# Kernel tuning notes

Hardware: AMD Instinct MI355X
Metric: run time of the kernel (lower is better)

## Reference

```python
import jax, jax.numpy as jnp
import numpy as np

N_NODES = 100000
N_EDGES = 1600000
N_REL = 8
IN_CH = 64
HIDDEN = 64
OUT_CH = 32


def setup_inputs() -> dict:
    key = jax.random.key(0)
    ks = jax.random.split(key, 10)
    s_in = 1.0 / np.sqrt(IN_CH)
    s_h = 1.0 / np.sqrt(HIDDEN)
    return {
        "x": jax.random.normal(ks[0], (N_NODES, IN_CH), dtype=jnp.float32),
        "edge_index": jax.random.randint(ks[1], (2, N_EDGES), 0, N_NODES, dtype=jnp.int64),
        "edge_type": jax.random.randint(ks[2], (N_EDGES,), 0, N_REL, dtype=jnp.int64),
        "W0": jax.random.normal(ks[3], (N_REL, IN_CH, HIDDEN), dtype=jnp.float32) * s_in,
        "Q0": jax.random.normal(ks[4], (HIDDEN, 1), dtype=jnp.float32) * s_h,
        "K0": jax.random.normal(ks[5], (HIDDEN, 1), dtype=jnp.float32) * s_h,
        "b0": jnp.zeros((HIDDEN,), dtype=jnp.float32),
        "W1": jax.random.normal(ks[6], (N_REL, HIDDEN, OUT_CH), dtype=jnp.float32) * s_h,
        "Q1": jax.random.normal(ks[7], (OUT_CH, 1), dtype=jnp.float32) * (1.0 / np.sqrt(OUT_CH)),
        "K1": jax.random.normal(ks[8], (OUT_CH, 1), dtype=jnp.float32) * (1.0 / np.sqrt(OUT_CH)),
        "b1": jnp.zeros((OUT_CH,), dtype=jnp.float32),
    }


def rgat_conv(x, src, dst, et, W, Q, K, b, n_nodes):
    # relation-typed transform of all nodes: [R, N, out]
    xw = jnp.einsum("ni,rio->rno", x, W)
    # per-node, per-relation attention logits (heads=1, dim=1)
    q = jnp.einsum("rno,od->rnd", xw, Q)[..., 0]  # [R, N]
    k = jnp.einsum("rno,od->rnd", xw, K)[..., 0]  # [R, N]
    # additive self-attention, leaky_relu slope 0.2 (PyG RGATConv default)
    alpha = jax.nn.leaky_relu(q[et, dst] + k[et, src], negative_slope=0.2)  # [E]
    # across-relation segment softmax over incoming edges of each dst node
    amax = jax.ops.segment_max(alpha, dst, num_segments=n_nodes)
    a = jnp.exp(alpha - amax[dst])
    denom = jax.ops.segment_sum(a, dst, num_segments=n_nodes)
    a = a / (denom[dst] + 1e-16)
    # weighted scatter-add aggregation of transformed source features
    msg = a[:, None] * xw[et, src]  # [E, out]
    return jax.ops.segment_sum(msg, dst, num_segments=n_nodes) + b


def reference(x, edge_index, edge_type, W0, Q0, K0, b0, W1, Q1, K1, b1):
    src, dst = edge_index[0], edge_index[1]
    n = x.shape[0]
    h = rgat_conv(x, src, dst, edge_type, W0, Q0, K0, b0, n)
    h = jax.nn.relu(h)  # dropout p=0.0 -> identity
    out = rgat_conv(h, src, dst, edge_type, W1, Q1, K1, b1, n)
    return out
```

## Files before the change

### kernel.cpp

```cpp
#include <hip/hip_runtime.h>
#include <hip/hip_bf16.h>
#include <math.h>


#define CSR_CHUNK 8192

__global__ void k_bhist(const int* __restrict__ dst, int* __restrict__ bcount,
                        int E, int NB) {
    __shared__ int h[512];
    int t = threadIdx.x;
    for (int i = t; i < NB; i += 256) h[i] = 0;
    __syncthreads();
    int e0 = blockIdx.x * CSR_CHUNK;
    int e1 = min(e0 + CSR_CHUNK, E);
    for (int i = e0 + t; i < e1; i += 256) atomicAdd(&h[dst[i] >> 8], 1);
    __syncthreads();
    for (int i = t; i < NB; i += 256) {
        int c = h[i];
        if (c) atomicAdd(&bcount[i], c);
    }
}

__global__ void k_bscan(const int* __restrict__ bcount, int* __restrict__ bstart,
                        int* __restrict__ gcur, int* __restrict__ rowptr,
                        int NB, int N, int E) {
    __shared__ int s[512];
    int t = threadIdx.x;
    int v = (t < NB) ? bcount[t] : 0;
    s[t] = v;
    __syncthreads();
    for (int off = 1; off < 512; off <<= 1) {
        int a = (t >= off) ? s[t - off] : 0;
        __syncthreads();
        s[t] += a;
        __syncthreads();
    }
    int excl = s[t] - v;
    if (t < NB) {
        bstart[t] = excl;
        gcur[t] = excl;
    }
    if (t == 0) {
        bstart[NB] = E;
        rowptr[N] = E;
    }
}

__global__ void k_bscatter(const int* __restrict__ src, const int* __restrict__ dst,
                           const int* __restrict__ et, int* __restrict__ gcur,
                           unsigned* __restrict__ ebuf, int E, int NB) {
    __shared__ int h[512];
    __shared__ int basearr[512];
    int t = threadIdx.x;
    for (int i = t; i < NB; i += 256) h[i] = 0;
    __syncthreads();
    int e0 = blockIdx.x * CSR_CHUNK;
    int e1 = min(e0 + CSR_CHUNK, E);
    for (int i = e0 + t; i < e1; i += 256) atomicAdd(&h[dst[i] >> 8], 1);
    __syncthreads();
    for (int i = t; i < NB; i += 256) {
        int c = h[i];
        basearr[i] = c ? atomicAdd(&gcur[i], c) : 0;
        h[i] = 0;
    }
    __syncthreads();
    for (int i = e0 + t; i < e1; i += 256) {
        int d = dst[i];
        int b = d >> 8;
        int off = atomicAdd(&h[b], 1);
        ebuf[basearr[b] + off] =
            ((unsigned)(d & 255) << 20) | ((unsigned)et[i] << 17) | (unsigned)src[i];
    }
}

__global__ void k_bsort(const unsigned* __restrict__ ebuf, const int* __restrict__ bstart,
                        int* __restrict__ rowptr, int* __restrict__ csr, int N) {
    __shared__ int lh[2048];
    __shared__ int ls[2048];
    __shared__ int ss[256];
    int b = blockIdx.x, t = threadIdx.x;
    int e0 = bstart[b], e1 = bstart[b + 1];
    for (int i = t; i < 2048; i += 256) lh[i] = 0;
    __syncthreads();
    for (int i = e0 + t; i < e1; i += 256) {
        unsigned u = ebuf[i];
        atomicAdd(&lh[(int)(((u >> 20) & 255) * 8 + ((u >> 17) & 7))], 1);
    }
    __syncthreads();
    int loc[8];
    int s = 0;
#pragma unroll
    for (int j = 0; j < 8; j++) {
        loc[j] = s;
        s += lh[t * 8 + j];
    }
    ss[t] = s;
    __syncthreads();
    for (int off = 1; off < 256; off <<= 1) {
        int a = (t >= off) ? ss[t - off] : 0;
        __syncthreads();
        ss[t] += a;
        __syncthreads();
    }
    int excl = ss[t] - s;
#pragma unroll
    for (int j = 0; j < 8; j++) ls[t * 8 + j] = excl + loc[j];
    int node = b * 256 + t;
    if (node < N) rowptr[node] = e0 + excl;
    __syncthreads();
    for (int i = t; i < 2048; i += 256) lh[i] = 0;
    __syncthreads();
    for (int i = e0 + t; i < e1; i += 256) {
        unsigned u = ebuf[i];
        int key = (int)(((u >> 20) & 255) * 8 + ((u >> 17) & 7));
        int off = atomicAdd(&lh[key], 1);
        csr[e0 + ls[key] + off] = (int)(u & 0xFFFFF);
    }
}


__global__ void k_wt2(const float* __restrict__ W, __hip_bfloat16* __restrict__ hi,
                      __hip_bfloat16* __restrict__ lo, int OUT, int total) {
    int t = blockIdx.x * blockDim.x + threadIdx.x;
    if (t < total) {
        int per = 64 * OUT;
        int r = t / per;
        int rem = t % per;
        int i = rem / OUT;
        int o = rem % OUT;
        float v = W[t];
        __hip_bfloat16 h = __float2bfloat16(v);
        __hip_bfloat16 l = __float2bfloat16(v - __bfloat162float(h));
        size_t idx = (size_t)o * 512 + i * 8 + r;
        hi[idx] = h;
        lo[idx] = l;
    }
}

__global__ void k_wqk(const float* W, const float* Qv, const float* Kv,
                      float* wq, float* wk, int OUT) {
    int t = blockIdx.x * blockDim.x + threadIdx.x;
    if (t < 8 * 64) {
        int r = t >> 6, i = t & 63;
        const float* wrow = W + ((size_t)r * 64 + i) * OUT;
        float a = 0.f, b = 0.f;
        for (int o = 0; o < OUT; o++) {
            float w = wrow[o];
            a += w * Qv[o];
            b += w * Kv[o];
        }
        wq[t] = a;
        wk[t] = b;
    }
}

__global__ __launch_bounds__(256) void k_qk2(
        const float* __restrict__ xin, const float* __restrict__ wq,
        const float* __restrict__ wk, float* __restrict__ qn,
        float* __restrict__ kn, unsigned short* __restrict__ xbb, int N) {
    __shared__ float xt[64][65];
    __shared__ float swq[8 * 65], swk[8 * 65];
    int t = threadIdx.x;
    int nb0 = blockIdx.x * 64;
    for (int i = t; i < 512; i += 256) {
        int r = i >> 6, c = i & 63;
        swq[r * 65 + c] = wq[i];
        swk[r * 65 + c] = wk[i];
    }
    for (int i = t; i < 1024; i += 256) {
        int ns = i >> 4;
        int c4 = i & 15;
        int n = nb0 + ns;
        float4 v = {0.f, 0.f, 0.f, 0.f};
        if (n < N) v = ((const float4*)xin)[(size_t)n * 16 + c4];
        xt[ns][c4 * 4 + 0] = v.x;
        xt[ns][c4 * 4 + 1] = v.y;
        xt[ns][c4 * 4 + 2] = v.z;
        xt[ns][c4 * 4 + 3] = v.w;
        if (n < N) {
            __hip_bfloat16 b0 = __float2bfloat16(v.x);
            __hip_bfloat16 b1 = __float2bfloat16(v.y);
            __hip_bfloat16 b2 = __float2bfloat16(v.z);
            __hip_bfloat16 b3 = __float2bfloat16(v.w);
            ushort4 o;
            o.x = *(unsigned short*)&b0;
            o.y = *(unsigned short*)&b1;
            o.z = *(unsigned short*)&b2;
            o.w = *(unsigned short*)&b3;
            *(ushort4*)(xbb + (size_t)n * 64 + c4 * 4) = o;
        }
    }
    __syncthreads();
#pragma unroll
    for (int g = t; g < 512; g += 256) {
        int ns = g >> 3, r = g & 7;
        int n = nb0 + ns;
        if (n < N) {
            float qa = 0.f, ka = 0.f;
#pragma unroll
            for (int i = 0; i < 64; i++) {
                float xv = xt[ns][i];
                qa += xv * swq[r * 65 + i];
                ka += xv * swk[r * 65 + i];
            }
            qn[(size_t)n * 8 + r] = qa;
            kn[(size_t)n * 8 + r] = ka;
        }
    }
}

#define ZSTR 520
template <int OUT, bool RELU>
__global__ __launch_bounds__(256) void k_fused(
        const int* __restrict__ rowptr, const int* __restrict__ csr,
        const float* __restrict__ qn, const float* __restrict__ kn,
        const unsigned short* __restrict__ xb,
        const __hip_bfloat16* __restrict__ wthi,
        const __hip_bfloat16* __restrict__ wtlo,
        const float* __restrict__ bias, float* __restrict__ xout, int N) {
    using v8s = __attribute__((ext_vector_type(8))) short;
    using v4f = __attribute__((ext_vector_type(4))) float;
    __shared__ unsigned short zt[16 * ZSTR];
    int wv = threadIdx.x >> 6;
    int lane = threadIdx.x & 63;
    int nb0 = blockIdx.x * 16;

    for (int q = 0; q < 4; q++) {
        int nl = wv * 4 + q;
        int wid = nb0 + nl;
        uint4 pack = {0u, 0u, 0u, 0u};
        if (wid < N) {
            int r0 = rowptr[wid], r1 = rowptr[wid + 1];
            float qv = (lane < 8) ? qn[wid * 8 + lane] : 0.f;
            float denom = 0.f;
            float a0 = 0.f, a1 = 0.f, a2 = 0.f, a3 = 0.f;
            float a4 = 0.f, a5 = 0.f, a6 = 0.f, a7 = 0.f;
            int currel = 0;
            float racc = 0.f;

            for (int base = r0; base < r1; base += 64) {
                int s = base + lane;
                int pk = (s < r1) ? csr[s] : 0;
                int src = pk & 0x1FFFF;
                int rel = pk >> 17;
                float qq = __shfl(qv, rel, 64);
                float tv = 0.f;
                if (s < r1) {
                    float v = qq + kn[src * 8 + rel];
                    v = (v >= 0.f) ? v : 0.2f * v;
                    tv = __expf(v);
                }
                float ts = tv;
#pragma unroll
                for (int off = 32; off > 0; off >>= 1) ts += __shfl_xor(ts, off, 64);
                denom += ts;

                int cnt = min(64, r1 - base);
                int tvi = (int)__float_as_uint(tv);
                for (int j = 0; j < cnt; j += 16) {
                    unsigned p[16];
                    float t[16];
#pragma unroll
                    for (int u = 0; u < 16; u++) {
                        p[u] = (unsigned)__builtin_amdgcn_readlane(pk, j + u);
                        t[u] = __uint_as_float(
                            (unsigned)__builtin_amdgcn_readlane(tvi, j + u));
                    }
                    unsigned xu[16];
#pragma unroll
                    for (int u = 0; u < 16; u++)
                        xu[u] = (unsigned)xb[(size_t)(p[u] & 0x1FFFF) * 64 + lane];
#pragma unroll
                    for (int u = 0; u < 16; u++) {
                        int rl = (int)(p[u] >> 17);
                        if (rl != currel) {
                            switch (currel) {
                                case 0: a0 += racc; break;
                                case 1: a1 += racc; break;
                                case 2: a2 += racc; break;
                                case 3: a3 += racc; break;
                                case 4: a4 += racc; break;
                                case 5: a5 += racc; break;
                                case 6: a6 += racc; break;
                                case 7: a7 += racc; break;
                            }
                            currel = rl;
                            racc = 0.f;
                        }
                        racc += t[u] * __uint_as_float(xu[u] << 16);
                    }
                }
            }
            switch (currel) {
                case 0: a0 += racc; break;
                case 1: a1 += racc; break;
                case 2: a2 += racc; break;
                case 3: a3 += racc; break;
                case 4: a4 += racc; break;
                case 5: a5 += racc; break;
                case 6: a6 += racc; break;
                case 7: a7 += racc; break;
            }
            float inv = 1.f / (denom + 1e-16f);
            float av[8] = {a0, a1, a2, a3, a4, a5, a6, a7};
            unsigned short u[8];
#pragma unroll
            for (int r = 0; r < 8; r++) {
                __hip_bfloat16 b = __float2bfloat16(av[r] * inv);
                u[r] = *(unsigned short*)&b;
            }
            pack.x = (unsigned)u[0] | ((unsigned)u[1] << 16);
            pack.y = (unsigned)u[2] | ((unsigned)u[3] << 16);
            pack.z = (unsigned)u[4] | ((unsigned)u[5] << 16);
            pack.w = (unsigned)u[6] | ((unsigned)u[7] << 16);
        }
        *(uint4*)&zt[nl * ZSTR + lane * 8] = pack;
    }
    __syncthreads();

    int quad = lane >> 4;
    int l15 = lane & 15;
    int nt = wv;
    if (nt * 16 < OUT) {
        const short* wh = (const short*)wthi;
        const short* wl = (const short*)wtlo;
        v4f acc = {0.f, 0.f, 0.f, 0.f};
#pragma unroll
        for (int k0 = 0; k0 < 512; k0 += 32) {
            int koff = k0 + quad * 8;
            v8s A = *(const v8s*)&zt[l15 * ZSTR + koff];
            v8s bh = *(const v8s*)(wh + (size_t)(nt * 16 + l15) * 512 + koff);
            v8s bl = *(const v8s*)(wl + (size_t)(nt * 16 + l15) * 512 + koff);
            acc = __builtin_amdgcn_mfma_f32_16x16x32_bf16(A, bh, acc, 0, 0, 0);
            acc = __builtin_amdgcn_mfma_f32_16x16x32_bf16(A, bl, acc, 0, 0, 0);
        }
        float bcol = bias[nt * 16 + l15];
#pragma unroll
        for (int g = 0; g < 4; g++) {
            int row = nb0 + quad * 4 + g;
            if (row < N) {
                float o = acc[g] + bcol;
                if (RELU) o = fmaxf(o, 0.f);
                xout[(size_t)row * OUT + nt * 16 + l15] = o;
            }
        }
    }
}


extern "C" void kernel_launch(void* const* d_in, const int* in_sizes, int n_in,
                              void* d_out, int out_size, void* d_ws, size_t ws_size,
                              hipStream_t stream) {
    const float* x   = (const float*)d_in[0];
    const int*   ei  = (const int*)d_in[1];
    const int*   et  = (const int*)d_in[2];
    const float* W0  = (const float*)d_in[3];
    const float* Q0  = (const float*)d_in[4];
    const float* K0  = (const float*)d_in[5];
    const float* b0  = (const float*)d_in[6];
    const float* W1  = (const float*)d_in[7];
    const float* Q1  = (const float*)d_in[8];
    const float* K1  = (const float*)d_in[9];
    const float* b1  = (const float*)d_in[10];
    float* out = (float*)d_out;

    const int N = in_sizes[0] / 64;
    const int E = in_sizes[2];
    const int* src = ei;
    const int* dst = ei + E;
    const int NB = (N + 255) >> 8;

    char* p = (char*)d_ws;
    auto alloc = [&](size_t bytes) -> void* {
        void* r = (void*)p;
        p += ((bytes + 255) / 256) * 256;
        return r;
    };
    int* rowptr   = (int*)alloc((size_t)(N + 1) * 4);
    int* bcount   = (int*)alloc(513 * 4);
    int* bstart   = (int*)alloc(513 * 4);
    int* gcur     = (int*)alloc(513 * 4);
    unsigned* ebuf = (unsigned*)alloc((size_t)E * 4);
    int* csr      = (int*)alloc((size_t)E * 4);
    float* wq     = (float*)alloc(8 * 64 * 4);
    float* wk     = (float*)alloc(8 * 64 * 4);
    float* qn     = (float*)alloc((size_t)N * 8 * 4);
    float* kn     = (float*)alloc((size_t)N * 8 * 4);
    __hip_bfloat16* wthi = (__hip_bfloat16*)alloc((size_t)64 * 512 * 2);
    __hip_bfloat16* wtlo = (__hip_bfloat16*)alloc((size_t)64 * 512 * 2);
    float* h      = (float*)alloc((size_t)N * 64 * 4);
    unsigned short* xbb = (unsigned short*)alloc((size_t)N * 64 * 2);

    int nchunks = (E + CSR_CHUNK - 1) / CSR_CHUNK;
    hipMemsetAsync(bcount, 0, (size_t)NB * 4, stream);
    k_bhist<<<nchunks, 256, 0, stream>>>(dst, bcount, E, NB);
    k_bscan<<<1, 512, 0, stream>>>(bcount, bstart, gcur, rowptr, NB, N, E);
    k_bscatter<<<nchunks, 256, 0, stream>>>(src, dst, et, gcur, ebuf, E, NB);
    k_bsort<<<NB, 256, 0, stream>>>(ebuf, bstart, rowptr, csr, N);

    int nfb = (N + 15) / 16;
    int nqkb = (N + 63) / 64;

    k_wqk<<<2, 256, 0, stream>>>(W0, Q0, K0, wq, wk, 64);
    k_qk2<<<nqkb, 256, 0, stream>>>(x, wq, wk, qn, kn, xbb, N);
    k_wt2<<<(8 * 64 * 64 + 255) / 256, 256, 0, stream>>>(W0, wthi, wtlo, 64, 8 * 64 * 64);
    k_fused<64, true><<<nfb, 256, 0, stream>>>(rowptr, csr, qn, kn, xbb,
                                               wthi, wtlo, b0, h, N);

    k_wqk<<<2, 256, 0, stream>>>(W1, Q1, K1, wq, wk, 32);
    k_qk2<<<nqkb, 256, 0, stream>>>(h, wq, wk, qn, kn, xbb, N);
    k_wt2<<<(8 * 64 * 32 + 255) / 256, 256, 0, stream>>>(W1, wthi, wtlo, 32, 8 * 64 * 32);
    k_fused<32, false><<<nfb, 256, 0, stream>>>(rowptr, csr, qn, kn, xbb,
                                                wthi, wtlo, b1, out, N);
}
```

Measured before the change: 444.9 us.

## Precompute block edge attention weights cooperatively into shared memory before gather

Adds a fast path for 16-node blocks with at most 512 edges. All 256 threads first compute the per-edge attention exponentials and pack them into shared memory, locating each edge's node by binary search over the rowptr slice. Per-node denominators are accumulated with shared-memory atomics. The gather loop then reads the weights uniformly from LDS, so the per-wave 64-edge chunking, reductions and readlanes go away. Blocks with more than 512 edges fall back to the old path. The cost is extra LDS, two more barriers and shared atomics on the denominators.

```diff
diff --git a/kernel.cpp b/kernel.cpp
--- a/kernel.cpp
+++ b/kernel.cpp
@@ -210,6 +210,22 @@
 }
 
 #define ZSTR 520
+#define EMAX 512
+
+#define FLUSH8()                          \
+    do {                                  \
+        switch (currel) {                 \
+            case 0: a0 += racc; break;    \
+            case 1: a1 += racc; break;    \
+            case 2: a2 += racc; break;    \
+            case 3: a3 += racc; break;    \
+            case 4: a4 += racc; break;    \
+            case 5: a5 += racc; break;    \
+            case 6: a6 += racc; break;    \
+            case 7: a7 += racc; break;    \
+        }                                 \
+    } while (0)
+
 template <int OUT, bool RELU>
 __global__ __launch_bounds__(256) void k_fused(
         const int* __restrict__ rowptr, const int* __restrict__ csr,
@@ -221,100 +237,175 @@
     using v8s = __attribute__((ext_vector_type(8))) short;
     using v4f = __attribute__((ext_vector_type(4))) float;
     __shared__ unsigned short zt[16 * ZSTR];
-    int wv = threadIdx.x >> 6;
-    int lane = threadIdx.x & 63;
+    __shared__ uint2 s_rec[EMAX];
+    __shared__ int s_rp[17];
+    __shared__ float s_q[128];
+    __shared__ float s_den[16];
+    int t = threadIdx.x;
+    int wv = t >> 6;
+    int lane = t & 63;
     int nb0 = blockIdx.x * 16;
 
-    for (int q = 0; q < 4; q++) {
-        int nl = wv * 4 + q;
-        int wid = nb0 + nl;
-        uint4 pack = {0u, 0u, 0u, 0u};
-        if (wid < N) {
-            int r0 = rowptr[wid], r1 = rowptr[wid + 1];
-            float qv = (lane < 8) ? qn[wid * 8 + lane] : 0.f;
-            float denom = 0.f;
+    if (t < 17) {
+        int nd = nb0 + t;
+        s_rp[t] = rowptr[nd > N ? N : nd];
+    }
+    if (t < 128) {
+        int nd = nb0 + (t >> 3);
+        s_q[t] = (nd < N) ? qn[(size_t)nd * 8 + (t & 7)] : 0.f;
+    }
+    if (t < 16) s_den[t] = 0.f;
+    __syncthreads();
+    int e0 = s_rp[0];
+    int esz = s_rp[16] - e0;
+
+    if (esz <= EMAX) {
+        for (int i = t; i < esz; i += 256) {
+            int ge = e0 + i;
+            int pk = csr[ge];
+            int lo = 0;
+            lo = (s_rp[lo + 8] <= ge) ? lo + 8 : lo;
+            lo = (s_rp[lo + 4] <= ge) ? lo + 4 : lo;
+            lo = (s_rp[lo + 2] <= ge) ? lo + 2 : lo;
+            lo = (s_rp[lo + 1] <= ge) ? lo + 1 : lo;
+            int rel = pk >> 17;
+            int src = pk & 0x1FFFF;
+            float v = s_q[lo * 8 + rel] + kn[(size_t)src * 8 + rel];
+            v = (v >= 0.f) ? v : 0.2f * v;
+            float tv = __expf(v);
+            atomicAdd(&s_den[lo], tv);
+            s_rec[i] = uint2{__float_as_uint(tv), (unsigned)pk};
+        }
+        __syncthreads();
+
+#pragma unroll 1
+        for (int q = 0; q < 4; q++) {
+            int nl = wv * 4 + q;
+            int r0 = s_rp[nl] - e0;
+            int r1 = s_rp[nl + 1] - e0;
             float a0 = 0.f, a1 = 0.f, a2 = 0.f, a3 = 0.f;
             float a4 = 0.f, a5 = 0.f, a6 = 0.f, a7 = 0.f;
             int currel = 0;
             float racc = 0.f;
-
-            for (int base = r0; base < r1; base += 64) {
-                int s = base + lane;
-                int pk = (s < r1) ? csr[s] : 0;
-                int src = pk & 0x1FFFF;
-                int rel = pk >> 17;
-                float qq = __shfl(qv, rel, 64);
-                float tv = 0.f;
-                if (s < r1) {
-                    float v = qq + kn[src * 8 + rel];
-                    v = (v >= 0.f) ? v : 0.2f * v;
-                    tv = __expf(v);
+#pragma unroll 1
+            for (int j = r0; j < r1; j += 16) {
+                float tvv[16];
+                int pkk[16];
+#pragma unroll
+                for (int u = 0; u < 16; u++) {
+                    int ii = j + u;
+                    bool ok = ii < r1;
+                    ii = ok ? ii : (r1 - 1);
+                    uint2 rc = s_rec[ii];
+                    tvv[u] = __uint_as_float(
+                        __builtin_amdgcn_readfirstlane((int)(ok ? rc.x : 0u)));
+                    pkk[u] = __builtin_amdgcn_readfirstlane((int)rc.y);
                 }
-                float ts = tv;
-#pragma unroll
-                for (int off = 32; off > 0; off >>= 1) ts += __shfl_xor(ts, off, 64);
-                denom += ts;
-
-                int cnt = min(64, r1 - base);
-                int tvi = (int)__float_as_uint(tv);
-                for (int j = 0; j < cnt; j += 16) {
-                    unsigned p[16];
-                    float t[16];
-#pragma unroll
-                    for (int u = 0; u < 16; u++) {
-                        p[u] = (unsigned)__builtin_amdgcn_readlane(pk, j + u);
-                        t[u] = __uint_as_float(
-                            (unsigned)__builtin_amdgcn_readlane(tvi, j + u));
+                unsigned short xu[16];
+#pragma unroll
+                for (int u = 0; u < 16; u++)
+                    xu[u] = xb[(size_t)(pkk[u] & 0x1FFFF) * 64 + lane];
+#pragma unroll
+                for (int u = 0; u < 16; u++) {
+                    int rl = pkk[u] >> 17;
+                    if (rl != currel) {
+                        FLUSH8();
+                        currel = rl;
+                        racc = 0.f;
                     }
-                    unsigned xu[16];
-#pragma unroll
-                    for (int u = 0; u < 16; u++)
-                        xu[u] = (unsigned)xb[(size_t)(p[u] & 0x1FFFF) * 64 + lane];
-#pragma unroll
-                    for (int u = 0; u < 16; u++) {
-                        int rl = (int)(p[u] >> 17);
-                        if (rl != currel) {
-                            switch (currel) {
-                                case 0: a0 += racc; break;
-                                case 1: a1 += racc; break;
-                                case 2: a2 += racc; break;
-                                case 3: a3 += racc; break;
-                                case 4: a4 += racc; break;
-                                case 5: a5 += racc; break;
-                                case 6: a6 += racc; break;
-                                case 7: a7 += racc; break;
+                    racc += tvv[u] * __uint_as_float(((unsigned)xu[u]) << 16);
+                }
+            }
+            FLUSH8();
+            float inv = 1.f / (s_den[nl] + 1e-16f);
+            float av[8] = {a0, a1, a2, a3, a4, a5, a6, a7};
+            unsigned short us[8];
+#pragma unroll
+            for (int r = 0; r < 8; r++) {
+                __hip_bfloat16 b = __float2bfloat16(av[r] * inv);
+                us[r] = *(unsigned short*)&b;
+            }
+            uint4 pack;
+            pack.x = (unsigned)us[0] | ((unsigned)us[1] << 16);
+            pack.y = (unsigned)us[2] | ((unsigned)us[3] << 16);
+            pack.z = (unsigned)us[4] | ((unsigned)us[5] << 16);
+            pack.w = (unsigned)us[6] | ((unsigned)us[7] << 16);
+            *(uint4*)&zt[nl * ZSTR + lane * 8] = pack;
+        }
+    } else {
+        for (int q = 0; q < 4; q++) {
+            int nl = wv * 4 + q;
+            int wid = nb0 + nl;
+            uint4 pack = {0u, 0u, 0u, 0u};
+            if (wid < N) {
+                int r0 = rowptr[wid], r1 = rowptr[wid + 1];
+                float qv = (lane < 8) ? qn[wid * 8 + lane] : 0.f;
+                float denom = 0.f;
+                float a0 = 0.f, a1 = 0.f, a2 = 0.f, a3 = 0.f;
+                float a4 = 0.f, a5 = 0.f, a6 = 0.f, a7 = 0.f;
+                int currel = 0;
+                float racc = 0.f;
+
+                for (int base = r0; base < r1; base += 64) {
+                    int s = base + lane;
+                    int pk = (s < r1) ? csr[s] : 0;
+                    int src = pk & 0x1FFFF;
+                    int rel = pk >> 17;
+                    float qq = __shfl(qv, rel, 64);
+                    float tv = 0.f;
+                    if (s < r1) {
+                        float v = qq + kn[src * 8 + rel];
+                        v = (v >= 0.f) ? v : 0.2f * v;
+                        tv = __expf(v);
+                    }
+                    float ts = tv;
+#pragma unroll
+                    for (int off = 32; off > 0; off >>= 1) ts += __shfl_xor(ts, off, 64);
+                    denom += ts;
+
+                    int cnt = min(64, r1 - base);
+                    int tvi = (int)__float_as_uint(tv);
+                    for (int j = 0; j < cnt; j += 16) {
+                        unsigned p[16];
+                        float tf[16];
+#pragma unroll
+                        for (int u = 0; u < 16; u++) {
+                            p[u] = (unsigned)__builtin_amdgcn_readlane(pk, j + u);
+                            tf[u] = __uint_as_float(
+                                (unsigned)__builtin_amdgcn_readlane(tvi, j + u));
+                        }
+                        unsigned xg[16];
+#pragma unroll
+                        for (int u = 0; u < 16; u++)
+                            xg[u] = (unsigned)xb[(size_t)(p[u] & 0x1FFFF) * 64 + lane];
+#pragma unroll
+                        for (int u = 0; u < 16; u++) {
+                            int rl = (int)(p[u] >> 17);
+                            if (rl != currel) {
+                                FLUSH8();
+                                currel = rl;
+                                racc = 0.f;
                             }
-                            currel = rl;
-                            racc = 0.f;
+                            racc += tf[u] * __uint_as_float(xg[u] << 16);
                         }
-                        racc += t[u] * __uint_as_float(xu[u] << 16);
                     }
                 }
+                FLUSH8();
+                float inv = 1.f / (denom + 1e-16f);
+                float av[8] = {a0, a1, a2, a3, a4, a5, a6, a7};
+                unsigned short us[8];
+#pragma unroll
+                for (int r = 0; r < 8; r++) {
+                    __hip_bfloat16 b = __float2bfloat16(av[r] * inv);
+                    us[r] = *(unsigned short*)&b;
+                }
+                pack.x = (unsigned)us[0] | ((unsigned)us[1] << 16);
+                pack.y = (unsigned)us[2] | ((unsigned)us[3] << 16);
+                pack.z = (unsigned)us[4] | ((unsigned)us[5] << 16);
+                pack.w = (unsigned)us[6] | ((unsigned)us[7] << 16);
             }
-            switch (currel) {
-                case 0: a0 += racc; break;
-                case 1: a1 += racc; break;
-                case 2: a2 += racc; break;
-                case 3: a3 += racc; break;
-                case 4: a4 += racc; break;
-                case 5: a5 += racc; break;
-                case 6: a6 += racc; break;
-                case 7: a7 += racc; break;
-            }
-            float inv = 1.f / (denom + 1e-16f);
-            float av[8] = {a0, a1, a2, a3, a4, a5, a6, a7};
-            unsigned short u[8];
-#pragma unroll
-            for (int r = 0; r < 8; r++) {
-                __hip_bfloat16 b = __float2bfloat16(av[r] * inv);
-                u[r] = *(unsigned short*)&b;
-            }
-            pack.x = (unsigned)u[0] | ((unsigned)u[1] << 16);
-            pack.y = (unsigned)u[2] | ((unsigned)u[3] << 16);
-            pack.z = (unsigned)u[4] | ((unsigned)u[5] << 16);
-            pack.w = (unsigned)u[6] | ((unsigned)u[7] << 16);
-        }
-        *(uint4*)&zt[nl * ZSTR + lane * 8] = pack;
+            *(uint4*)&zt[nl * ZSTR + lane * 8] = pack;
+        }
     }
     __syncthreads();
 
```

Result: no change. 438.3 us, median of 2 (-1.5%).

## Compute attention scores per edge uniformly in gather loop instead of lane-parallel batch

Applied to the files above, without the earlier changes.

The per-node aggregation loop drops the 64-lane batched attention computation with cross-lane reductions and readlane broadcasts. It now reads 16 CSR entries as uniform (scalar) loads, fetches their k values, and computes the exp weights redundantly in every lane alongside the feature gather. The denominator is accumulated inline, so the shuffle reductions go away. The CSR build now stores the full packed word, and the zero-fill of the tile moves to the start so out-of-range waves can exit early. The cost is redundant per-lane exp and k loads; the gain is fewer cross-lane operations and less serialization on low-degree nodes.

```diff
diff --git a/kernel.cpp b/kernel.cpp
--- a/kernel.cpp
+++ b/kernel.cpp
@@ -114,7 +114,7 @@
         unsigned u = ebuf[i];
         int key = (int)(((u >> 20) & 255) * 8 + ((u >> 17) & 7));
         int off = atomicAdd(&lh[key], 1);
-        csr[e0 + ls[key] + off] = (int)(u & 0xFFFFF);
+        csr[e0 + ls[key] + off] = (int)u;
     }
 }
 
@@ -210,6 +210,21 @@
 }
 
 #define ZSTR 520
+
+#define FLUSH8()                          \
+    do {                                  \
+        switch (currel) {                 \
+            case 0: a0 += racc; break;    \
+            case 1: a1 += racc; break;    \
+            case 2: a2 += racc; break;    \
+            case 3: a3 += racc; break;    \
+            case 4: a4 += racc; break;    \
+            case 5: a5 += racc; break;    \
+            case 6: a6 += racc; break;    \
+            case 7: a7 += racc; break;    \
+        }                                 \
+    } while (0)
+
 template <int OUT, bool RELU>
 __global__ __launch_bounds__(256) void k_fused(
         const int* __restrict__ rowptr, const int* __restrict__ csr,
@@ -221,106 +236,89 @@
     using v8s = __attribute__((ext_vector_type(8))) short;
     using v4f = __attribute__((ext_vector_type(4))) float;
     __shared__ unsigned short zt[16 * ZSTR];
-    int wv = threadIdx.x >> 6;
-    int lane = threadIdx.x & 63;
+    int t = threadIdx.x;
+    int wvu = __builtin_amdgcn_readfirstlane(t >> 6);
+    int lane = t & 63;
     int nb0 = blockIdx.x * 16;
 
+    {
+        uint4 zz = {0u, 0u, 0u, 0u};
+#pragma unroll
+        for (int q = 0; q < 4; q++)
+            *(uint4*)&zt[(wvu * 4 + q) * ZSTR + lane * 8] = zz;
+    }
+
+#pragma unroll 1
     for (int q = 0; q < 4; q++) {
-        int nl = wv * 4 + q;
-        int wid = nb0 + nl;
-        uint4 pack = {0u, 0u, 0u, 0u};
-        if (wid < N) {
-            int r0 = rowptr[wid], r1 = rowptr[wid + 1];
-            float qv = (lane < 8) ? qn[wid * 8 + lane] : 0.f;
-            float denom = 0.f;
-            float a0 = 0.f, a1 = 0.f, a2 = 0.f, a3 = 0.f;
-            float a4 = 0.f, a5 = 0.f, a6 = 0.f, a7 = 0.f;
-            int currel = 0;
-            float racc = 0.f;
-
-            for (int base = r0; base < r1; base += 64) {
-                int s = base + lane;
-                int pk = (s < r1) ? csr[s] : 0;
-                int src = pk & 0x1FFFF;
-                int rel = pk >> 17;
-                float qq = __shfl(qv, rel, 64);
-                float tv = 0.f;
-                if (s < r1) {
-                    float v = qq + kn[src * 8 + rel];
-                    v = (v >= 0.f) ? v : 0.2f * v;
-                    tv = __expf(v);
+        int wid = nb0 + wvu * 4 + q;
+        if (wid >= N) break;
+        int r0 = rowptr[wid];
+        int r1 = rowptr[wid + 1];
+        int qvec = 0;
+        if (lane < 8) qvec = ((const int*)qn)[wid * 8 + lane];
+
+        float a0 = 0.f, a1 = 0.f, a2 = 0.f, a3 = 0.f;
+        float a4 = 0.f, a5 = 0.f, a6 = 0.f, a7 = 0.f;
+        float racc = 0.f, denom = 0.f;
+        int currel = 0;
+
+#pragma unroll 1
+        for (int j = r0; j < r1; j += 16) {
+            int pk[16];
+            float kv[16];
+            unsigned short xu[16];
+#pragma unroll
+            for (int u = 0; u < 16; u++) {
+                int ii = (j + u < r1) ? (j + u) : (r1 - 1);
+                pk[u] = csr[ii];
+            }
+#pragma unroll
+            for (int u = 0; u < 16; u++) {
+                int s_ = pk[u] & 0x1FFFF;
+                int r_ = (pk[u] >> 17) & 7;
+                kv[u] = kn[(size_t)s_ * 8 + r_];
+            }
+#pragma unroll
+            for (int u = 0; u < 16; u++)
+                xu[u] = xb[(size_t)(pk[u] & 0x1FFFF) * 64 + lane];
+#pragma unroll
+            for (int u = 0; u < 16; u++) {
+                int rl = (pk[u] >> 17) & 7;
+                float qv = __uint_as_float(__builtin_amdgcn_readlane(qvec, rl));
+                float v = qv + kv[u];
+                v = fmaxf(v, 0.2f * v);
+                float tv = __expf(v);
+                if (j + u >= r1) tv = 0.f;
+                if (rl != currel) {
+                    FLUSH8();
+                    currel = rl;
+                    racc = 0.f;
                 }
-                float ts = tv;
-#pragma unroll
-                for (int off = 32; off > 0; off >>= 1) ts += __shfl_xor(ts, off, 64);
-                denom += ts;
-
-                int cnt = min(64, r1 - base);
-                int tvi = (int)__float_as_uint(tv);
-                for (int j = 0; j < cnt; j += 16) {
-                    unsigned p[16];
-                    float t[16];
-#pragma unroll
-                    for (int u = 0; u < 16; u++) {
-                        p[u] = (unsigned)__builtin_amdgcn_readlane(pk, j + u);
-                        t[u] = __uint_as_float(
-                            (unsigned)__builtin_amdgcn_readlane(tvi, j + u));
-                    }
-                    unsigned xu[16];
-#pragma unroll
-                    for (int u = 0; u < 16; u++)
-                        xu[u] = (unsigned)xb[(size_t)(p[u] & 0x1FFFF) * 64 + lane];
-#pragma unroll
-                    for (int u = 0; u < 16; u++) {
-                        int rl = (int)(p[u] >> 17);
-                        if (rl != currel) {
-                            switch (currel) {
-                                case 0: a0 += racc; break;
-                                case 1: a1 += racc; break;
-                                case 2: a2 += racc; break;
-                                case 3: a3 += racc; break;
-                                case 4: a4 += racc; break;
-                                case 5: a5 += racc; break;
-                                case 6: a6 += racc; break;
-                                case 7: a7 += racc; break;
-                            }
-                            currel = rl;
-                            racc = 0.f;
-                        }
-                        racc += t[u] * __uint_as_float(xu[u] << 16);
-                    }
-                }
+                racc += tv * __uint_as_float(((unsigned)xu[u]) << 16);
+                denom += tv;
             }
-            switch (currel) {
-                case 0: a0 += racc; break;
-                case 1: a1 += racc; break;
-                case 2: a2 += racc; break;
-                case 3: a3 += racc; break;
-                case 4: a4 += racc; break;
-                case 5: a5 += racc; break;
-                case 6: a6 += racc; break;
-                case 7: a7 += racc; break;
-            }
-            float inv = 1.f / (denom + 1e-16f);
-            float av[8] = {a0, a1, a2, a3, a4, a5, a6, a7};
-            unsigned short u[8];
-#pragma unroll
-            for (int r = 0; r < 8; r++) {
-                __hip_bfloat16 b = __float2bfloat16(av[r] * inv);
-                u[r] = *(unsigned short*)&b;
-            }
-            pack.x = (unsigned)u[0] | ((unsigned)u[1] << 16);
-            pack.y = (unsigned)u[2] | ((unsigned)u[3] << 16);
-            pack.z = (unsigned)u[4] | ((unsigned)u[5] << 16);
-            pack.w = (unsigned)u[6] | ((unsigned)u[7] << 16);
-        }
-        *(uint4*)&zt[nl * ZSTR + lane * 8] = pack;
+        }
+        FLUSH8();
+        float inv = 1.f / (denom + 1e-16f);
+        float av[8] = {a0, a1, a2, a3, a4, a5, a6, a7};
+        unsigned short us[8];
+#pragma unroll
+        for (int r = 0; r < 8; r++) {
+            __hip_bfloat16 b = __float2bfloat16(av[r] * inv);
+            us[r] = *(unsigned short*)&b;
+        }
+        uint4 pack;
+        pack.x = (unsigned)us[0] | ((unsigned)us[1] << 16);
+        pack.y = (unsigned)us[2] | ((unsigned)us[3] << 16);
+        pack.z = (unsigned)us[4] | ((unsigned)us[5] << 16);
+        pack.w = (unsigned)us[6] | ((unsigned)us[7] << 16);
+        *(uint4*)&zt[(wvu * 4 + q) * ZSTR + lane * 8] = pack;
     }
     __syncthreads();
 
     int quad = lane >> 4;
     int l15 = lane & 15;
-    int nt = wv;
+    int nt = wvu;
     if (nt * 16 < OUT) {
         const short* wh = (const short*)wthi;
         const short* wl = (const short*)wtlo;
```

Result: slower. 474.3 us (+6.6%).
